# Kernel optimization log

Hardware: AMD Instinct MI355X
Metric: run time of the kernel (lower is better)

## Reference

```python
import jax, jax.numpy as jnp
import numpy as np

B, T, E, H, LBL = 32, 2048, 256, 256, 20


def _lstm_cell_step(x, W_ih, b_ih, b_hh):
    # Single LSTM cell step from zero state (h0=c0=0): W_hh @ h0 == 0.
    # x: [B, T, E]; W_ih: [4H, E]; gate order in torch: i, f, g, o
    gates = jnp.einsum('bte,ge->btg', x, W_ih) + b_ih + b_hh  # [B, T, 4H]
    i, f, g, o = jnp.split(gates, 4, axis=-1)
    c = jax.nn.sigmoid(i) * jnp.tanh(g)  # f * c0 == 0
    return jax.nn.sigmoid(o) * jnp.tanh(c)  # [B, T, H]


def setup_inputs() -> dict:
    key = jax.random.key(0)
    ks = jax.random.split(key, 12)
    s_ih = 1.0 / np.sqrt(H)
    inp = {
        'X': jax.random.normal(ks[0], (B, T, E), dtype=jnp.float32),
        'lengths': jax.random.randint(ks[1], (B,), 1, T + 1, dtype=jnp.int32),
        'W_ih_f': jax.random.uniform(ks[2], (4 * H, E), jnp.float32, -s_ih, s_ih),
        'b_ih_f': jax.random.uniform(ks[3], (4 * H,), jnp.float32, -s_ih, s_ih),
        'b_hh_f': jax.random.uniform(ks[4], (4 * H,), jnp.float32, -s_ih, s_ih),
        'W_ih_r': jax.random.uniform(ks[5], (4 * H, E), jnp.float32, -s_ih, s_ih),
        'b_ih_r': jax.random.uniform(ks[6], (4 * H,), jnp.float32, -s_ih, s_ih),
        'b_hh_r': jax.random.uniform(ks[7], (4 * H,), jnp.float32, -s_ih, s_ih),
        'W1': jax.random.uniform(ks[8], (256, 4 * H), jnp.float32, -1 / np.sqrt(4 * H), 1 / np.sqrt(4 * H)),
        'b1': jax.random.uniform(ks[9], (256,), jnp.float32, -1 / np.sqrt(4 * H), 1 / np.sqrt(4 * H)),
        'W2': jax.random.uniform(ks[10], (LBL, 256), jnp.float32, -1 / 16.0, 1 / 16.0),
        'b2': jax.random.uniform(ks[11], (LBL,), jnp.float32, -1 / 16.0, 1 / 16.0),
    }
    return inp


def reference(X, lengths, W_ih_f, b_ih_f, b_hh_f, W_ih_r, b_ih_r, b_hh_r, W1, b1, W2, b2):
    lengths = jnp.clip(lengths, 1, T).astype(jnp.int32)
    # Both directions are independent single-step cells (seq_len==1 in original)
    h_f = _lstm_cell_step(X, W_ih_f, b_ih_f, b_hh_f)  # [B, T, H]
    h_r = _lstm_cell_step(X, W_ih_r, b_ih_r, b_hh_r)  # [B, T, H]
    s = jnp.concatenate([h_f, h_r], axis=-1)          # [B, T, 2H]
    mask = (jnp.arange(T)[None, :] < lengths[:, None])  # [B, T]
    m = mask[:, :, None].astype(s.dtype)
    avg_pool = (s * m).sum(axis=1) / lengths[:, None].astype(s.dtype)  # [B, 2H]
    NEG = jnp.asarray(-1e30, s.dtype)
    max_pool = jnp.where(mask[:, :, None], s, NEG).max(axis=1)          # [B, 2H]
    doc = jnp.concatenate([avg_pool, max_pool], axis=-1)                # [B, 4H]
    rel = jax.nn.relu(doc)
    d1 = rel @ W1.T + b1        # dropout is identity in eval mode
    return d1 @ W2.T + b2        # [B, LBL]
```

## Files before the change

kernel.cpp:

```cpp
#include <hip/hip_runtime.h>
#include <stdint.h>

#define B_   32
#define T_   2048
#define E_   256
#define H_   256
#define LBL_ 20
#define M_   (B_ * T_)
#define NPACK_ 1536

typedef __attribute__((ext_vector_type(8))) short bf16x8;
typedef __attribute__((ext_vector_type(4))) float f32x4;

__device__ __forceinline__ unsigned short f2bf(float f) {
    union { float f; unsigned int u; } a; a.f = f;
    unsigned int u = a.u;
    u += 0x7FFFu + ((u >> 16) & 1u);
    return (unsigned short)(u >> 16);
}

__device__ __forceinline__ float rcp_(float x) {
#if __has_builtin(__builtin_amdgcn_rcpf)
    return __builtin_amdgcn_rcpf(x);
#else
    return 1.0f / x;
#endif
}
__device__ __forceinline__ float exp2_(float x) {
#if __has_builtin(__builtin_amdgcn_exp2f)
    return __builtin_amdgcn_exp2f(x);
#else
    return exp2f(x);
#endif
}

__global__ __launch_bounds__(256) void prep(
    const float4* __restrict__ X4, uint4* __restrict__ Xb4,
    const int* __restrict__ lengths,
    const float* __restrict__ Wf, const float* __restrict__ bif, const float* __restrict__ bhf,
    const float* __restrict__ Wr, const float* __restrict__ bir, const float* __restrict__ bhr,
    unsigned short* __restrict__ Wp, float* __restrict__ bias_p)
{
    int bi = blockIdx.x;
    if (bi < 8192) {
        int b = bi >> 8, tile = bi & 255;
        int lenb = lengths[b]; lenb = lenb < 1 ? 1 : (lenb > T_ ? T_ : lenb);
        int used = (lenb + 127) & ~127;
        if (tile * 8 >= used) return;
        int idx = b * 65536 + tile * 256 + threadIdx.x;
        float4 v0 = X4[2 * idx], v1 = X4[2 * idx + 1];
        union { unsigned short us[8]; uint4 u; } r;
        r.us[0] = f2bf(v0.x); r.us[1] = f2bf(v0.y); r.us[2] = f2bf(v0.z); r.us[3] = f2bf(v0.w);
        r.us[4] = f2bf(v1.x); r.us[5] = f2bf(v1.y); r.us[6] = f2bf(v1.z); r.us[7] = f2bf(v1.w);
        Xb4[idx] = r.u;
    } else {
        int n = bi - 8192, t = threadIdx.x;
        int gidx = n / 48, r = n % 48;
        int ty = r >> 4, cc = r & 15;
        int dir = gidx >> 4, c = (gidx & 15) * 16 + cc;
        int gate = (ty == 0) ? 0 : (ty == 1 ? 2 : 3);
        int wrow = gate * 256 + c;
        const float* W = dir ? Wr : Wf;
        Wp[n * 256 + t] = f2bf(W[wrow * 256 + t]);
        if (t == 0)
            bias_p[n] = (dir ? bir[wrow] : bif[wrow]) + (dir ? bhr[wrow] : bhf[wrow]);
    }
}

__global__ __launch_bounds__(256, 3) void gemm_pool(
    const unsigned short* __restrict__ Xb, const unsigned short* __restrict__ Wp,
    const float* __restrict__ bias_p, const int* __restrict__ lengths,
    float* __restrict__ psum, float* __restrict__ pmax)
{
    __shared__ __align__(16) short Bs[96 * 256];
    __shared__ float red[2][4][2][16];

    const int tid  = threadIdx.x;
    const int w    = tid >> 6;
    const int lane = tid & 63;
    const int g    = blockIdx.x;
    const int m_tile = ((g >> 7) << 3) + (g & 7);
    const int n_tile = (g >> 3) & 15;
    const int m0   = m_tile << 7;
    const int n0   = n_tile * 96;

    const int b  = m0 >> 11;
    const int t0 = m0 & 2047;
    int lenb = lengths[b]; lenb = lenb < 1 ? 1 : (lenb > T_ ? T_ : lenb);

    if (t0 >= lenb) return;

    #pragma unroll
    for (int rr = 0; rr < 12; ++rr) {
        int s = rr * 256 + tid;
        int row = s >> 5, kcs = s & 31;
        int kc = (kcs & 24) | ((kcs & 7) ^ (row & 7));
        __builtin_amdgcn_global_load_lds(
            (const __attribute__((address_space(1))) void*)(Wp + (n0 + row) * 256 + kc * 8),
            (__attribute__((address_space(3))) void*)(Bs + (rr * 256 + (w << 6)) * 8),
            16, 0, 0);
    }

    f32x4 acc[2][6];
    #pragma unroll
    for (int i = 0; i < 2; ++i)
        #pragma unroll
        for (int j = 0; j < 6; ++j) acc[i][j] = (f32x4){0.f, 0.f, 0.f, 0.f};

    const int rowa = m0 + w * 32 + (lane & 15);
    const int q    = lane >> 4;
    const unsigned short* Abase = Xb + rowa * 256 + q * 8;

    bf16x8 aU[4], aV[4];
    #pragma unroll
    for (int ks = 0; ks < 2; ++ks)
        #pragma unroll
        for (int rt = 0; rt < 2; ++rt)
            aU[ks * 2 + rt] = *(const bf16x8*)(Abase + rt * 16 * 256 + ks * 4 * 8);

    __syncthreads();

    #pragma unroll
    for (int kit = 0; kit < 4; ++kit) {
        bf16x8* cur = (kit & 1) ? aV : aU;
        bf16x8* nxt = (kit & 1) ? aU : aV;
        if (kit < 3) {
            #pragma unroll
            for (int ks = 0; ks < 2; ++ks)
                #pragma unroll
                for (int rt = 0; rt < 2; ++rt)
                    nxt[ks * 2 + rt] = *(const bf16x8*)(Abase + rt * 16 * 256
                                                        + ((kit + 1) * 8 + ks * 4) * 8);
        }
        #pragma unroll
        for (int ks = 0; ks < 2; ++ks) {
            bf16x8 bfr[6];
            int kc = kit * 8 + ks * 4 + q;
            #pragma unroll
            for (int ct = 0; ct < 6; ++ct) {
                int rb = ct * 16 + (lane & 15);
                int slot = rb * 32 + (kc & 24) + ((kc & 7) ^ (rb & 7));
                bfr[ct] = *(const bf16x8*)(Bs + slot * 8);
            }
            #pragma unroll
            for (int rt = 0; rt < 2; ++rt)
                #pragma unroll
                for (int ct = 0; ct < 6; ++ct)
                    acc[rt][ct] = __builtin_amdgcn_mfma_f32_16x16x32_bf16(
                        cur[ks * 2 + rt], bfr[ct], acc[rt][ct], 0, 0, 0);
        }
    }

    const int cc = lane & 15;
    const float L2E = 1.44269504f;

    #pragma unroll
    for (int gg = 0; gg < 2; ++gg) {
        float bi = bias_p[n0 + gg * 48 + 0  + cc];
        float bg = bias_p[n0 + gg * 48 + 16 + cc];
        float bo = bias_p[n0 + gg * 48 + 32 + cc];
        float hsum = 0.f, hmax = -1e30f;
        #pragma unroll
        for (int rt = 0; rt < 2; ++rt) {
            if (t0 + w * 32 + rt * 16 >= lenb) continue;
            #pragma unroll
            for (int reg = 0; reg < 4; ++reg) {
                int row = w * 32 + rt * 16 + q * 4 + reg;
                int t = t0 + row;
                float iv = acc[rt][gg * 3 + 0][reg] + bi;
                float gv = acc[rt][gg * 3 + 1][reg] + bg;
                float ov = acc[rt][gg * 3 + 2][reg] + bo;
                float e1 = exp2_(iv * -L2E);
                float e2 = exp2_(gv * -2.f * L2E);
                float e3 = exp2_(ov * -L2E);
                float cv = (1.f - e2) * rcp_((1.f + e1) * (1.f + e2));
                float tt  = cv * cv;
                float num = cv * __builtin_fmaf(tt, tt + 105.f, 945.f);
                float den = __builtin_fmaf(tt, __builtin_fmaf(tt, 15.f, 420.f), 945.f);
                float h = num * rcp_(den * (1.f + e3));
                if (t < lenb) { hsum += h; hmax = fmaxf(hmax, h); }
            }
        }
        hsum += __shfl_xor(hsum, 16, 64);
        hmax = fmaxf(hmax, __shfl_xor(hmax, 16, 64));
        hsum += __shfl_xor(hsum, 32, 64);
        hmax = fmaxf(hmax, __shfl_xor(hmax, 32, 64));
        if (q == 0) { red[0][w][gg][cc] = hsum; red[1][w][gg][cc] = hmax; }
    }
    __syncthreads();
    if (tid < 32) {
        int gg = tid >> 4, c16 = tid & 15;
        float s  = red[0][0][gg][c16] + red[0][1][gg][c16] + red[0][2][gg][c16] + red[0][3][gg][c16];
        float mx = fmaxf(fmaxf(red[1][0][gg][c16], red[1][1][gg][c16]),
                         fmaxf(red[1][2][gg][c16], red[1][3][gg][c16]));
        int gidx = n_tile * 2 + gg;
        int col2 = (gidx >> 4) * 256 + (gidx & 15) * 16 + c16;
        int mt = m_tile & 15;
        psum[(b * 16 + mt) * 512 + col2] = s;
        pmax[(b * 16 + mt) * 512 + col2] = mx;
    }
}

__global__ __launch_bounds__(256) void mlp1(
    const float* __restrict__ psum, const float* __restrict__ pmax,
    const int* __restrict__ lengths,
    const float* __restrict__ W1, const float* __restrict__ b1,
    float* __restrict__ d1g)
{
    __shared__ float doc[1024];
    int nt = blockIdx.x, b = blockIdx.y, tid = threadIdx.x;
    int lenb = lengths[b]; lenb = lenb < 1 ? 1 : (lenb > T_ ? T_ : lenb);
    int cnt = (lenb + 127) >> 7;
    float invlen = 1.f / (float)lenb;
    for (int col = tid; col < 512; col += 256) {
        float s = 0.f, mx = -1e30f;
        for (int mt = 0; mt < cnt; ++mt) {
            s += psum[(b * 16 + mt) * 512 + col];
            mx = fmaxf(mx, pmax[(b * 16 + mt) * 512 + col]);
        }
        doc[col]       = fmaxf(s * invlen, 0.f);
        doc[512 + col] = fmaxf(mx, 0.f);
    }
    __syncthreads();
    int neuron = tid >> 2, tq = tid & 3;
    int row = nt * 64 + neuron;
    const float4* wrow = (const float4*)(W1 + row * 1024 + tq * 256);
    const float4* dv   = (const float4*)doc + tq * 64;
    float a0 = 0.f, a1 = 0.f, a2 = 0.f, a3 = 0.f;
    #pragma unroll 4
    for (int k = 0; k < 64; ++k) {
        float4 wv = wrow[k]; float4 xv = dv[k];
        a0 += wv.x * xv.x; a1 += wv.y * xv.y; a2 += wv.z * xv.z; a3 += wv.w * xv.w;
    }
    float a = a0 + a1 + a2 + a3;
    a += __shfl_xor(a, 1, 64);
    a += __shfl_xor(a, 2, 64);
    if (tq == 0) d1g[b * 256 + row] = a + b1[row];
}

__global__ __launch_bounds__(256) void mlp2(
    const float* __restrict__ d1g,
    const float* __restrict__ W2, const float* __restrict__ b2,
    float* __restrict__ out)
{
    __shared__ float d1s[256];
    int b = blockIdx.x, tid = threadIdx.x;
    d1s[tid] = d1g[b * 256 + tid];
    __syncthreads();
    int j = tid >> 3, tq = tid & 7;
    float a = 0.f;
    if (j < LBL_) {
        const float4* wr = (const float4*)(W2 + j * 256) + tq * 8;
        const float4* dd = (const float4*)d1s + tq * 8;
        #pragma unroll
        for (int k = 0; k < 8; ++k) {
            float4 wv = wr[k]; float4 xv = dd[k];
            a += wv.x * xv.x + wv.y * xv.y + wv.z * xv.z + wv.w * xv.w;
        }
    }
    a += __shfl_xor(a, 1, 64);
    a += __shfl_xor(a, 2, 64);
    a += __shfl_xor(a, 4, 64);
    if (j < LBL_ && tq == 0) out[b * LBL_ + j] = a + b2[j];
}

#define XB_OFF   0u
#define WP_OFF   33554432u
#define BIAS_OFF 34340864u
#define PSUM_OFF 34347008u
#define PMAX_OFF 35395584u
#define D1_OFF   36444160u

extern "C" void kernel_launch(void* const* d_in, const int* in_sizes, int n_in,
                              void* d_out, int out_size, void* d_ws, size_t ws_size,
                              hipStream_t stream) {
    (void)in_sizes; (void)n_in; (void)out_size; (void)ws_size;
    const float* X      = (const float*)d_in[0];
    const int*   lens   = (const int*)d_in[1];
    const float* W_ih_f = (const float*)d_in[2];
    const float* b_ih_f = (const float*)d_in[3];
    const float* b_hh_f = (const float*)d_in[4];
    const float* W_ih_r = (const float*)d_in[5];
    const float* b_ih_r = (const float*)d_in[6];
    const float* b_hh_r = (const float*)d_in[7];
    const float* W1     = (const float*)d_in[8];
    const float* b1     = (const float*)d_in[9];
    const float* W2     = (const float*)d_in[10];
    const float* b2     = (const float*)d_in[11];
    float* out = (float*)d_out;

    char* ws = (char*)d_ws;
    unsigned short* Xb     = (unsigned short*)(ws + XB_OFF);
    unsigned short* Wp     = (unsigned short*)(ws + WP_OFF);
    float*          bias_p = (float*)(ws + BIAS_OFF);
    float*          psum   = (float*)(ws + PSUM_OFF);
    float*          pmax   = (float*)(ws + PMAX_OFF);
    float*          d1g    = (float*)(ws + D1_OFF);

    prep<<<dim3(8192 + NPACK_), 256, 0, stream>>>(
        (const float4*)X, (uint4*)Xb, lens,
        W_ih_f, b_ih_f, b_hh_f, W_ih_r, b_ih_r, b_hh_r, Wp, bias_p);
    gemm_pool<<<dim3(8192), 256, 0, stream>>>(Xb, Wp, bias_p, lens, psum, pmax);
    mlp1<<<dim3(4, 32), 256, 0, stream>>>(psum, pmax, lens, W1, b1, d1g);
    mlp2<<<dim3(B_), 256, 0, stream>>>(d1g, W2, b2, out);
}
```

Before: 204.2 us.

## Make gemm_pool persistent over a compacted list of live M tiles

The prep kernel gains an extra block that builds a compact list of valid (batch, tile) items from the sequence lengths. gemm_pool now launches a fixed grid of 768 blocks (48 workers per N tile) that loop over this list. Each block loads its weight slice into LDS once and prefetches the next tile's A fragments across iterations. This is meant to remove launch and exit overhead from the many early-returning blocks and to reuse the LDS weight tile, at the cost of load imbalance and a serial list-building block inside prep.

After: 176.1 us. -13.8%, faster.

```diff
diff --git a/kernel.cpp b/kernel.cpp
--- a/kernel.cpp
+++ b/kernel.cpp
@@ -39,7 +39,8 @@
     const int* __restrict__ lengths,
     const float* __restrict__ Wf, const float* __restrict__ bif, const float* __restrict__ bhf,
     const float* __restrict__ Wr, const float* __restrict__ bir, const float* __restrict__ bhr,
-    unsigned short* __restrict__ Wp, float* __restrict__ bias_p)
+    unsigned short* __restrict__ Wp, float* __restrict__ bias_p,
+    int* __restrict__ live)
 {
     int bi = blockIdx.x;
     if (bi < 8192) {
@@ -53,7 +54,7 @@
         r.us[0] = f2bf(v0.x); r.us[1] = f2bf(v0.y); r.us[2] = f2bf(v0.z); r.us[3] = f2bf(v0.w);
         r.us[4] = f2bf(v1.x); r.us[5] = f2bf(v1.y); r.us[6] = f2bf(v1.z); r.us[7] = f2bf(v1.w);
         Xb4[idx] = r.u;
-    } else {
+    } else if (bi < 8192 + NPACK_) {
         int n = bi - 8192, t = threadIdx.x;
         int gidx = n / 48, r = n % 48;
         int ty = r >> 4, cc = r & 15;
@@ -64,31 +65,45 @@
         Wp[n * 256 + t] = f2bf(W[wrow * 256 + t]);
         if (t == 0)
             bias_p[n] = (dir ? bir[wrow] : bif[wrow]) + (dir ? bhr[wrow] : bhf[wrow]);
+    } else {
+        __shared__ int cnts[32], offs[32], lens[32];
+        int t = threadIdx.x;
+        if (t < 32) {
+            int lenb = lengths[t]; lenb = lenb < 1 ? 1 : (lenb > T_ ? T_ : lenb);
+            lens[t] = lenb;
+            cnts[t] = (lenb + 127) >> 7;
+        }
+        __syncthreads();
+        if (t == 0) {
+            int acc = 0;
+            for (int b = 0; b < 32; ++b) { offs[b] = acc; acc += cnts[b]; }
+            live[0] = acc;
+        }
+        __syncthreads();
+        if (t < 32) {
+            int o = offs[t], lenb = lens[t];
+            for (int k = 0; k < cnts[t]; ++k)
+                live[1 + o + k] = (lenb << 9) | (t * 16 + k);
+        }
     }
 }
 
 __global__ __launch_bounds__(256, 3) void gemm_pool(
     const unsigned short* __restrict__ Xb, const unsigned short* __restrict__ Wp,
-    const float* __restrict__ bias_p, const int* __restrict__ lengths,
+    const float* __restrict__ bias_p, const int* __restrict__ live,
     float* __restrict__ psum, float* __restrict__ pmax)
 {
     __shared__ __align__(16) short Bs[96 * 256];
-    __shared__ float red[2][4][2][16];
-
-    const int tid  = threadIdx.x;
-    const int w    = tid >> 6;
-    const int lane = tid & 63;
-    const int g    = blockIdx.x;
-    const int m_tile = ((g >> 7) << 3) + (g & 7);
-    const int n_tile = (g >> 3) & 15;
-    const int m0   = m_tile << 7;
-    const int n0   = n_tile * 96;
-
-    const int b  = m0 >> 11;
-    const int t0 = m0 & 2047;
-    int lenb = lengths[b]; lenb = lenb < 1 ? 1 : (lenb > T_ ? T_ : lenb);
-
-    if (t0 >= lenb) return;
+    __shared__ float red[2][4][2][16][2];
+
+    const int tid    = threadIdx.x;
+    const int w      = tid >> 6;
+    const int lane   = tid & 63;
+    const int n_tile = blockIdx.x & 15;
+    const int worker = blockIdx.x >> 4;
+    const int n0     = n_tile * 96;
+    const int q      = lane >> 4;
+    const int cc     = lane & 15;
 
     #pragma unroll
     for (int rr = 0; rr < 12; ++rr) {
@@ -101,103 +116,133 @@
             16, 0, 0);
     }
 
-    f32x4 acc[2][6];
+    float bI[2], bG[2], bO[2];
     #pragma unroll
-    for (int i = 0; i < 2; ++i)
-        #pragma unroll
-        for (int j = 0; j < 6; ++j) acc[i][j] = (f32x4){0.f, 0.f, 0.f, 0.f};
-
-    const int rowa = m0 + w * 32 + (lane & 15);
-    const int q    = lane >> 4;
-    const unsigned short* Abase = Xb + rowa * 256 + q * 8;
-
+    for (int gg = 0; gg < 2; ++gg) {
+        bI[gg] = bias_p[n0 + gg * 48 + 0  + cc];
+        bG[gg] = bias_p[n0 + gg * 48 + 16 + cc];
+        bO[gg] = bias_p[n0 + gg * 48 + 32 + cc];
+    }
+
+    const int nlive = live[0];
+    const int* list = live + 1;
+
+    int j = worker;
+    int item = (j < nlive) ? list[j] : -1;
+    const unsigned short* Ab = Xb;
     bf16x8 aU[4], aV[4];
-    #pragma unroll
-    for (int ks = 0; ks < 2; ++ks)
-        #pragma unroll
-        for (int rt = 0; rt < 2; ++rt)
-            aU[ks * 2 + rt] = *(const bf16x8*)(Abase + rt * 16 * 256 + ks * 4 * 8);
+    if (item >= 0) {
+        Ab = Xb + (((item & 511) << 7) + w * 32 + (lane & 15)) * 256 + q * 8;
+        #pragma unroll
+        for (int ks = 0; ks < 2; ++ks)
+            #pragma unroll
+            for (int rt = 0; rt < 2; ++rt)
+                aU[ks * 2 + rt] = *(const bf16x8*)(Ab + rt * 16 * 256 + ks * 4 * 8);
+    }
 
     __syncthreads();
 
-    #pragma unroll
-    for (int kit = 0; kit < 4; ++kit) {
-        bf16x8* cur = (kit & 1) ? aV : aU;
-        bf16x8* nxt = (kit & 1) ? aU : aV;
-        if (kit < 3) {
+    int par = 0;
+    const float L2E = 1.44269504f;
+
+    while (item >= 0) {
+        int jn = j + 48;
+        int itemn = (jn < nlive) ? list[jn] : -1;
+        const unsigned short* Abn = (itemn >= 0)
+            ? Xb + (((itemn & 511) << 7) + w * 32 + (lane & 15)) * 256 + q * 8
+            : Ab;
+
+        f32x4 acc[2][6];
+        #pragma unroll
+        for (int i = 0; i < 2; ++i)
             #pragma unroll
-            for (int ks = 0; ks < 2; ++ks)
-                #pragma unroll
-                for (int rt = 0; rt < 2; ++rt)
-                    nxt[ks * 2 + rt] = *(const bf16x8*)(Abase + rt * 16 * 256
-                                                        + ((kit + 1) * 8 + ks * 4) * 8);
-        }
-        #pragma unroll
-        for (int ks = 0; ks < 2; ++ks) {
-            bf16x8 bfr[6];
-            int kc = kit * 8 + ks * 4 + q;
-            #pragma unroll
-            for (int ct = 0; ct < 6; ++ct) {
-                int rb = ct * 16 + (lane & 15);
-                int slot = rb * 32 + (kc & 24) + ((kc & 7) ^ (rb & 7));
-                bfr[ct] = *(const bf16x8*)(Bs + slot * 8);
+            for (int jj = 0; jj < 6; ++jj) acc[i][jj] = (f32x4){0.f, 0.f, 0.f, 0.f};
+
+        #pragma unroll
+        for (int kit = 0; kit < 4; ++kit) {
+            bf16x8* cur = (kit & 1) ? aV : aU;
+            bf16x8* nxt = (kit & 1) ? aU : aV;
+            if (kit < 3) {
+                #pragma unroll
+                for (int ks = 0; ks < 2; ++ks)
+                    #pragma unroll
+                    for (int rt = 0; rt < 2; ++rt)
+                        nxt[ks * 2 + rt] = *(const bf16x8*)(Ab + rt * 16 * 256
+                                                            + ((kit + 1) * 8 + ks * 4) * 8);
+            } else {
+                #pragma unroll
+                for (int ks = 0; ks < 2; ++ks)
+                    #pragma unroll
+                    for (int rt = 0; rt < 2; ++rt)
+                        nxt[ks * 2 + rt] = *(const bf16x8*)(Abn + rt * 16 * 256 + ks * 4 * 8);
             }
             #pragma unroll
-            for (int rt = 0; rt < 2; ++rt)
-                #pragma unroll
-                for (int ct = 0; ct < 6; ++ct)
-                    acc[rt][ct] = __builtin_amdgcn_mfma_f32_16x16x32_bf16(
-                        cur[ks * 2 + rt], bfr[ct], acc[rt][ct], 0, 0, 0);
-        }
-    }
-
-    const int cc = lane & 15;
-    const float L2E = 1.44269504f;
-
-    #pragma unroll
-    for (int gg = 0; gg < 2; ++gg) {
-        float bi = bias_p[n0 + gg * 48 + 0  + cc];
-        float bg = bias_p[n0 + gg * 48 + 16 + cc];
-        float bo = bias_p[n0 + gg * 48 + 32 + cc];
-        float hsum = 0.f, hmax = -1e30f;
-        #pragma unroll
-        for (int rt = 0; rt < 2; ++rt) {
-            if (t0 + w * 32 + rt * 16 >= lenb) continue;
+            for (int ks = 0; ks < 2; ++ks) {
+                bf16x8 bfr[6];
+                int kc = kit * 8 + ks * 4 + q;
+                #pragma unroll
+                for (int ct = 0; ct < 6; ++ct) {
+                    int rb = ct * 16 + (lane & 15);
+                    int slot = rb * 32 + (kc & 24) + ((kc & 7) ^ (rb & 7));
+                    bfr[ct] = *(const bf16x8*)(Bs + slot * 8);
+                }
+                #pragma unroll
+                for (int rt = 0; rt < 2; ++rt)
+                    #pragma unroll
+                    for (int ct = 0; ct < 6; ++ct)
+                        acc[rt][ct] = __builtin_amdgcn_mfma_f32_16x16x32_bf16(
+                            cur[ks * 2 + rt], bfr[ct], acc[rt][ct], 0, 0, 0);
+            }
+        }
+
+        const int idx9 = item & 511;
+        const int lenb = item >> 9;
+        const int t0   = (idx9 & 15) << 7;
+
+        #pragma unroll
+        for (int gg = 0; gg < 2; ++gg) {
+            float hsum = 0.f, hmax = -1e30f;
             #pragma unroll
-            for (int reg = 0; reg < 4; ++reg) {
-                int row = w * 32 + rt * 16 + q * 4 + reg;
-                int t = t0 + row;
-                float iv = acc[rt][gg * 3 + 0][reg] + bi;
-                float gv = acc[rt][gg * 3 + 1][reg] + bg;
-                float ov = acc[rt][gg * 3 + 2][reg] + bo;
-                float e1 = exp2_(iv * -L2E);
-                float e2 = exp2_(gv * -2.f * L2E);
-                float e3 = exp2_(ov * -L2E);
-                float cv = (1.f - e2) * rcp_((1.f + e1) * (1.f + e2));
-                float tt  = cv * cv;
-                float num = cv * __builtin_fmaf(tt, tt + 105.f, 945.f);
-                float den = __builtin_fmaf(tt, __builtin_fmaf(tt, 15.f, 420.f), 945.f);
-                float h = num * rcp_(den * (1.f + e3));
-                if (t < lenb) { hsum += h; hmax = fmaxf(hmax, h); }
+            for (int rt = 0; rt < 2; ++rt) {
+                if (t0 + w * 32 + rt * 16 >= lenb) continue;
+                #pragma unroll
+                for (int reg = 0; reg < 4; ++reg) {
+                    int row = w * 32 + rt * 16 + q * 4 + reg;
+                    int t = t0 + row;
+                    float iv = acc[rt][gg * 3 + 0][reg] + bI[gg];
+                    float gv = acc[rt][gg * 3 + 1][reg] + bG[gg];
+                    float ov = acc[rt][gg * 3 + 2][reg] + bO[gg];
+                    float e1 = exp2_(iv * -L2E);
+                    float e2 = exp2_(gv * -2.f * L2E);
+                    float e3 = exp2_(ov * -L2E);
+                    float cv = (1.f - e2) * rcp_((1.f + e1) * (1.f + e2));
+                    float tt  = cv * cv;
+                    float num = cv * __builtin_fmaf(tt, tt + 105.f, 945.f);
+                    float den = __builtin_fmaf(tt, __builtin_fmaf(tt, 15.f, 420.f), 945.f);
+                    float h = num * rcp_(den * (1.f + e3));
+                    if (t < lenb) { hsum += h; hmax = fmaxf(hmax, h); }
+                }
             }
-        }
-        hsum += __shfl_xor(hsum, 16, 64);
-        hmax = fmaxf(hmax, __shfl_xor(hmax, 16, 64));
-        hsum += __shfl_xor(hsum, 32, 64);
-        hmax = fmaxf(hmax, __shfl_xor(hmax, 32, 64));
-        if (q == 0) { red[0][w][gg][cc] = hsum; red[1][w][gg][cc] = hmax; }
-    }
-    __syncthreads();
-    if (tid < 32) {
-        int gg = tid >> 4, c16 = tid & 15;
-        float s  = red[0][0][gg][c16] + red[0][1][gg][c16] + red[0][2][gg][c16] + red[0][3][gg][c16];
-        float mx = fmaxf(fmaxf(red[1][0][gg][c16], red[1][1][gg][c16]),
-                         fmaxf(red[1][2][gg][c16], red[1][3][gg][c16]));
-        int gidx = n_tile * 2 + gg;
-        int col2 = (gidx >> 4) * 256 + (gidx & 15) * 16 + c16;
-        int mt = m_tile & 15;
-        psum[(b * 16 + mt) * 512 + col2] = s;
-        pmax[(b * 16 + mt) * 512 + col2] = mx;
+            hsum += __shfl_xor(hsum, 16, 64);
+            hmax = fmaxf(hmax, __shfl_xor(hmax, 16, 64));
+            hsum += __shfl_xor(hsum, 32, 64);
+            hmax = fmaxf(hmax, __shfl_xor(hmax, 32, 64));
+            if (q == 0) { red[par][w][gg][cc][0] = hsum; red[par][w][gg][cc][1] = hmax; }
+        }
+        __syncthreads();
+        if (tid < 32) {
+            int gg = tid >> 4, c16 = tid & 15;
+            float s  = red[par][0][gg][c16][0] + red[par][1][gg][c16][0]
+                     + red[par][2][gg][c16][0] + red[par][3][gg][c16][0];
+            float mx = fmaxf(fmaxf(red[par][0][gg][c16][1], red[par][1][gg][c16][1]),
+                             fmaxf(red[par][2][gg][c16][1], red[par][3][gg][c16][1]));
+            int gidx = n_tile * 2 + gg;
+            int col2 = (gidx >> 4) * 256 + (gidx & 15) * 16 + c16;
+            psum[idx9 * 512 + col2] = s;
+            pmax[idx9 * 512 + col2] = mx;
+        }
+        par ^= 1;
+        j = jn; item = itemn; Ab = Abn;
     }
 }
 
@@ -270,6 +315,7 @@
 #define PSUM_OFF 34347008u
 #define PMAX_OFF 35395584u
 #define D1_OFF   36444160u
+#define LIVE_OFF 36476928u
 
 extern "C" void kernel_launch(void* const* d_in, const int* in_sizes, int n_in,
                               void* d_out, int out_size, void* d_ws, size_t ws_size,
@@ -296,11 +342,12 @@
     float*          psum   = (float*)(ws + PSUM_OFF);
     float*          pmax   = (float*)(ws + PMAX_OFF);
     float*          d1g    = (float*)(ws + D1_OFF);
-
-    prep<<<dim3(8192 + NPACK_), 256, 0, stream>>>(
+    int*            live   = (int*)(ws + LIVE_OFF);
+
+    prep<<<dim3(8192 + NPACK_ + 1), 256, 0, stream>>>(
         (const float4*)X, (uint4*)Xb, lens,
-        W_ih_f, b_ih_f, b_hh_f, W_ih_r, b_ih_r, b_hh_r, Wp, bias_p);
-    gemm_pool<<<dim3(8192), 256, 0, stream>>>(Xb, Wp, bias_p, lens, psum, pmax);
+        W_ih_f, b_ih_f, b_hh_f, W_ih_r, b_ih_r, b_hh_r, Wp, bias_p, live);
+    gemm_pool<<<dim3(768), 256, 0, stream>>>(Xb, Wp, bias_p, live, psum, pmax);
     mlp1<<<dim3(4, 32), 256, 0, stream>>>(psum, pmax, lens, W1, b1, d1g);
     mlp2<<<dim3(B_), 256, 0, stream>>>(d1g, W2, b2, out);
 }
```
